# Kernel tuning notes

Measured on AMD Instinct MI355X. Metric: run time of the kernel, lower is better.

The kernel has to match this reference:

```python
import jax, jax.numpy as jnp
import numpy as np

D_MODEL = 512
N_HEADS = 8
DH = D_MODEL // N_HEADS            # 64
Q_PROJ = D_MODEL // 2              # 256
KV_PROJ = (2 * D_MODEL) // 3       # 341
ROPE_DIM = D_MODEL // 8            # 64 total rope dims
R = ROPE_DIM // N_HEADS            # 8 rope dims per head
THETA = 10000.0
EPS = 1e-5
B, S = 2, 2048


def layernorm(x, g, b):
    m = jnp.mean(x, axis=-1, keepdims=True)
    v = jnp.var(x, axis=-1, keepdims=True)
    return (x - m) * jax.lax.rsqrt(v + EPS) * g + b


def rope_cos_sin(seq_len, dtype):
    inv_freq = THETA ** (-jnp.arange(0, R, 2, dtype=jnp.float32) / R)   # (R/2,)
    ang = jnp.arange(seq_len, dtype=jnp.float32)[:, None] * inv_freq   # (S, R/2)
    cos = jnp.concatenate([jnp.cos(ang), jnp.cos(ang)], axis=-1)        # (S, R)
    sin = jnp.concatenate([jnp.sin(ang), jnp.sin(ang)], axis=-1)
    return cos.astype(dtype), sin.astype(dtype)


def apply_rope(x, cos, sin):
    # x: (B, H, S, R); neox-style half rotation
    x1, x2 = jnp.split(x, 2, axis=-1)
    rot = jnp.concatenate([-x2, x1], axis=-1)
    return x * cos + rot * sin


def setup_inputs() -> dict:
    key = jax.random.key(0)
    ks = jax.random.split(key, 9)
    p = lambda k, shape: 0.01 * jax.random.normal(k, shape, jnp.float32)
    return {
        "x": jax.random.normal(ks[0], (B, S, D_MODEL), jnp.float32),
        "W_dq": p(ks[1], (D_MODEL, Q_PROJ)),
        "W_uq": p(ks[2], (Q_PROJ, D_MODEL)),
        "W_qr": p(ks[3], (Q_PROJ, ROPE_DIM)),
        "W_dkv": p(ks[4], (D_MODEL, KV_PROJ)),
        "W_ukv": p(ks[5], (KV_PROJ, 2 * D_MODEL)),
        "W_kr": p(ks[6], (D_MODEL, ROPE_DIM)),
        "W_o": p(ks[7], (D_MODEL, D_MODEL)),
        "q_ln_g": jnp.ones((Q_PROJ,), jnp.float32),
        "q_ln_b": jnp.zeros((Q_PROJ,), jnp.float32),
        "kv_ln_g": jnp.ones((KV_PROJ,), jnp.float32),
        "kv_ln_b": jnp.zeros((KV_PROJ,), jnp.float32),
    }


def reference(x, W_dq, W_uq, W_qr, W_dkv, W_ukv, W_kr, W_o,
              q_ln_g, q_ln_b, kv_ln_g, kv_ln_b):
    b, s, d = x.shape
    # --- low-rank Q path ---
    cq = layernorm(x @ W_dq, q_ln_g, q_ln_b)                      # (B,S,Q_PROJ)
    Q = (cq @ W_uq).reshape(b, s, N_HEADS, DH).transpose(0, 2, 1, 3)
    Qr = (cq @ W_qr).reshape(b, s, N_HEADS, R).transpose(0, 2, 1, 3)
    cos, sin = rope_cos_sin(s, x.dtype)
    Qr = apply_rope(Qr, cos, sin)
    q = jnp.concatenate([Q, Qr], axis=-1)                          # (B,H,S,DH+R)
    # --- low-rank KV path ---
    ckv = layernorm(x @ W_dkv, kv_ln_g, kv_ln_b)                  # (B,S,KV_PROJ)
    KV = ckv @ W_ukv                                              # (B,S,2*D)
    K, V = KV[..., :D_MODEL], KV[..., D_MODEL:]
    K = K.reshape(b, s, N_HEADS, DH).transpose(0, 2, 1, 3)
    Kr = (x @ W_kr).reshape(b, s, N_HEADS, R).transpose(0, 2, 1, 3)
    Kr = apply_rope(Kr, cos, sin)
    k = jnp.concatenate([K, Kr], axis=-1)                          # (B,H,S,DH+R)
    v = V.reshape(b, s, N_HEADS, DH).transpose(0, 2, 1, 3)         # (B,H,S,DH)
    # --- causal SDPA ---
    scale = 1.0 / jnp.sqrt(jnp.asarray(DH + R, x.dtype))
    scores = jnp.einsum('bhqd,bhkd->bhqk', q, k) * scale           # (B,H,S,S)
    mask = jnp.tril(jnp.ones((s, s), dtype=bool))
    scores = jnp.where(mask, scores, jnp.finfo(scores.dtype).min)
    attn = jax.nn.softmax(scores, axis=-1)
    out = jnp.einsum('bhqk,bhkd->bhqd', attn, v)
    out = out.transpose(0, 2, 1, 3).reshape(b, s, d)
    return out @ W_o.T, ckv
```

## Files before the change

kernel.cpp:

```cpp
#include <hip/hip_runtime.h>
#include <hip/hip_bf16.h>

#define BATCH 2
#define SEQ 2048
#define DM 512
#define NH 8
#define DHD 64
#define QP 256
#define KVP 341
#define DQKPAD 96
#define MROWS 4096

#define OFF_X     0
#define OFF_WO    2932224
#define OFF_QG    3194368
#define OFF_QB    3194624
#define OFF_KG    3194880
#define OFF_KB    3195221

#define T_DQ   0
#define T_DKV  131072
#define T_KR   327680
#define T_UQ   360448
#define T_QR   491520
#define T_UKV  507904
#define T_TOT  901120

#define NW_X   2097152
#define NW_WO  262144
#define NW_PAR 1194

#define G_X   262144
#define G_WO  32768
#define G_PAR 150
#define G_WT  112640
#define G_TOT (G_X + G_WO + G_PAR + G_WT)

#define NSPLIT 8

typedef __bf16 bf16x8 __attribute__((ext_vector_type(8)));
typedef float f32x4 __attribute__((ext_vector_type(4)));
typedef __hip_bfloat16 bf16;
typedef unsigned short u16;

static __device__ __forceinline__ bf16x8 ld_bf8(const bf16* p) {
    return __builtin_bit_cast(bf16x8, *(const uint4*)p);
}

#define GL16(gp, lp) __builtin_amdgcn_global_load_lds( \
    (const __attribute__((address_space(1))) void*)(gp), \
    (__attribute__((address_space(3))) void*)(lp), 16, 0, 0)

__global__ __launch_bounds__(256) void prep(
    const void* px, const void* pwdq, const void* pwuq, const void* pwqr,
    const void* pwdkv, const void* pwukv, const void* pwkr, const void* pwo,
    const void* pqg, const void* pqb, const void* pkg, const void* pkb,
    u16* __restrict__ arena, u16* __restrict__ WT, int* __restrict__ flagp)
{
    __shared__ int cnt;
    if (threadIdx.x == 0) cnt = 0;
    __syncthreads();
    int bad = 0;
    const u16* xs = (const u16*)px;
    for (int i = threadIdx.x; i < 2048; i += 256) {
        u16 u = xs[i];
        int e = (u >> 7) & 0xFF;
        if (u != 0 && (e < 90 || e > 164)) bad++;
    }
    #pragma unroll
    for (int m2 = 1; m2 < 64; m2 <<= 1) bad += __shfl_xor(bad, m2);
    if ((threadIdx.x & 63) == 0) atomicAdd(&cnt, bad);
    __syncthreads();
    const int f = (cnt > 256) ? 1 : 0;
    if (blockIdx.x == 0 && threadIdx.x == 0) *flagp = f;

    int gid = blockIdx.x * 256 + threadIdx.x;
    if (gid >= G_TOT) return;

    auto rdu = [&](const void* s, int i) -> u16 {
        if (f) return __builtin_bit_cast(u16, __float2bfloat16(((const float*)s)[i]));
        return ((const u16*)s)[i];
    };

    if (gid < G_X + G_WO) {
        const void* src = (gid < G_X) ? px : pwo;
        int base = (gid < G_X) ? OFF_X : OFF_WO;
        int i = (gid < G_X) ? gid : gid - G_X;
        u16 out[8];
        if (f) {
            const float* s = (const float*)src + i * 8;
            #pragma unroll
            for (int j = 0; j < 8; ++j) out[j] = __builtin_bit_cast(u16, __float2bfloat16(s[j]));
        } else {
            *(uint4*)out = ((const uint4*)src)[i];
        }
        *(uint4*)&arena[base + i * 8] = *(uint4*)out;
    } else if (gid < G_X + G_WO + G_PAR) {
        int i0 = (gid - G_X - G_WO) * 8;
        for (int j = 0; j < 8; ++j) {
            int i = i0 + j;
            if (i >= NW_PAR) break;
            if (i < 256)      arena[OFF_QG + i]         = rdu(pqg, i);
            else if (i < 512) arena[OFF_QB + (i - 256)] = rdu(pqb, i - 256);
            else if (i < 853) arena[OFF_KG + (i - 512)] = rdu(pkg, i - 512);
            else              arena[OFF_KB + (i - 853)] = rdu(pkb, i - 853);
        }
    } else {
        int loc = (gid - (G_X + G_WO + G_PAR)) * 8;
        const void* src; int n, k0, sN, klim, nok;
        if (loc < T_DKV)      { int l = loc;          n = l >> 9; k0 = l & 511; src = pwdq;  sN = 256;  klim = 512; nok = 1; }
        else if (loc < T_KR)  { int l = loc - T_DKV;  n = l >> 9; k0 = l & 511; src = pwdkv; sN = 341;  klim = 512; nok = (n < 341); }
        else if (loc < T_UQ)  { int l = loc - T_KR;   n = l >> 9; k0 = l & 511; src = pwkr;  sN = 64;   klim = 512; nok = 1; }
        else if (loc < T_QR)  { int l = loc - T_UQ;   n = l >> 8; k0 = l & 255; src = pwuq;  sN = 512;  klim = 256; nok = 1; }
        else if (loc < T_UKV) { int l = loc - T_QR;   n = l >> 8; k0 = l & 255; src = pwqr;  sN = 64;   klim = 256; nok = 1; }
        else                  { int l = loc - T_UKV;  n = l / 384; k0 = l % 384; src = pwukv; sN = 1024; klim = 341; nok = 1; }
        u16 out[8];
        #pragma unroll
        for (int j = 0; j < 8; ++j) {
            int k = k0 + j;
            out[j] = (nok && k < klim) ? rdu(src, k * sN + n) : (u16)0;
        }
        *(uint4*)&WT[loc] = *(uint4*)out;
    }
}

static __device__ __forceinline__ void rope_epi(
    f32x4 (&acc)[2][4], bf16* __restrict__ dst, int m0, int w, int g, int lr, int tid, bool scaleq)
{
    const float SCv = 0.11785113019775793f;
    #pragma unroll
    for (int mt = 0; mt < 2; ++mt)
    #pragma unroll
    for (int r = 0; r < 4; ++r) {
        int gm = m0 + w * 32 + mt * 16 + g * 4 + r;
        int s = gm & 2047, b = gm >> 11;
        float ang = (float)s * exp2f(-(float)(lr & 3) * 3.3219280948873623f);
        float sn, cs;
        sincosf(ang, &sn, &cs);
        #pragma unroll
        for (int nt = 0; nt < 4; ++nt) {
            float v = acc[mt][nt][r];
            float pt = __shfl_xor(v, 4);
            float o = (lr & 4) ? fmaf(pt, sn, v * cs) : fmaf(-pt, sn, v * cs);
            if (scaleq) o *= SCv;
            int h = (nt * 16 + lr) >> 3, j = lr & 7;
            dst[((size_t)(b * NH + h) * SEQ + s) * DQKPAD + 64 + j] = __float2bfloat16(o);
        }
    }
    for (int u = tid; u < 128 * 96; u += 256) {
        int rw = u / 96, rem = u - rw * 96;
        int h = rem / 12, c = rem - h * 12;
        int row = m0 + rw, b2 = row >> 11, s2 = row & 2047;
        *(unsigned int*)&dst[((size_t)(b2 * NH + h) * SEQ + s2) * DQKPAD + 72 + c * 2] = 0u;
    }
}

__global__ __launch_bounds__(256) void gemm128(
    const bf16* __restrict__ A, int lda,
    const bf16* __restrict__ BT, int ldb,
    int N, int Kpad, int mode,
    void* __restrict__ C0, int ldc,
    bf16* __restrict__ kv_k, bf16* __restrict__ kv_v,
    const int* __restrict__ flagp, float* __restrict__ C0f)
{
    __shared__ __align__(16) bf16 LB[128 * 64 + 64 * 64];
    bf16* Al = LB;
    bf16* Bl = LB + 128 * 64;
    const int tid = threadIdx.x;
    const int m0 = blockIdx.y * 128, n0 = blockIdx.x * 64;
    const int lane = tid & 63, w = tid >> 6;
    const int g = lane >> 4, lr = lane & 15;
    f32x4 acc[2][4] = {};
    const int r8 = lane >> 3;
    const int xr8 = ((lane & 7) ^ r8) * 8;
    const int swx = (lr & 7) << 4;

    for (int k0 = 0; k0 < Kpad; k0 += 64) {
        #pragma unroll
        for (int i = 0; i < 4; ++i)
            GL16(&A[(size_t)(m0 + w * 32 + i * 8 + r8) * lda + k0 + xr8],
                 (char*)Al + w * 4096 + i * 1024);
        #pragma unroll
        for (int i = 0; i < 2; ++i)
            GL16(&BT[(size_t)(n0 + w * 16 + i * 8 + r8) * ldb + k0 + xr8],
                 (char*)Bl + w * 2048 + i * 1024);
        __syncthreads();
        #pragma unroll
        for (int ks = 0; ks < 2; ++ks) {
            const int cs = (ks * 64 + g * 16) ^ swx;
            bf16x8 a0 = ld_bf8((const bf16*)((const char*)Al + (w * 32 + lr) * 128 + cs));
            bf16x8 a1 = ld_bf8((const bf16*)((const char*)Al + (w * 32 + 16 + lr) * 128 + cs));
            #pragma unroll
            for (int nt = 0; nt < 4; ++nt) {
                bf16x8 b = ld_bf8((const bf16*)((const char*)Bl + (nt * 16 + lr) * 128 + cs));
                acc[0][nt] = __builtin_amdgcn_mfma_f32_16x16x32_bf16(a0, b, acc[0][nt], 0, 0, 0);
                acc[1][nt] = __builtin_amdgcn_mfma_f32_16x16x32_bf16(a1, b, acc[1][nt], 0, 0, 0);
            }
        }
        __syncthreads();
    }

    if (mode == 0 && n0 == 640) {
        rope_epi(acc, kv_k, m0, w, g, lr, tid, false);
        return;
    }
    if (mode == 4 && n0 == DM) {
        rope_epi(acc, (bf16*)C0, m0, w, g, lr, tid, true);
        return;
    }
    if (mode == 3 && n0 >= DM) {
        const int h = (n0 - DM) >> 6;
        const int b = m0 >> 11, s0 = m0 & 2047;
        bf16* T = LB;
        #pragma unroll
        for (int mt = 0; mt < 2; ++mt)
        #pragma unroll
        for (int nt = 0; nt < 4; ++nt)
        #pragma unroll
        for (int r = 0; r < 4; ++r) {
            int dv = nt * 16 + lr;
            int sl = w * 32 + mt * 16 + g * 4 + r;
            T[dv * 136 + sl] = __float2bfloat16(acc[mt][nt][r]);
        }
        __syncthreads();
        const int row = tid >> 2, coff = (tid & 3) * 32;
        bf16* dst = &kv_v[((size_t)(b * NH + h) * DHD + row) * SEQ + s0 + coff];
        const bf16* srcp = &T[row * 136 + coff];
        #pragma unroll
        for (int q2 = 0; q2 < 4; ++q2)
            *(uint4*)(dst + q2 * 8) = *(const uint4*)(srcp + q2 * 8);
        return;
    }

    const float SCv = 0.11785113019775793f;
    const int f32o = (mode == 1 && flagp) ? *flagp : 0;
    #pragma unroll
    for (int mt = 0; mt < 2; ++mt)
    #pragma unroll
    for (int nt = 0; nt < 4; ++nt)
    #pragma unroll
    for (int r = 0; r < 4; ++r) {
        int gm = m0 + w * 32 + mt * 16 + g * 4 + r;
        int gn = n0 + nt * 16 + lr;
        float v = acc[mt][nt][r];
        if (mode == 0) {
            ((float*)C0)[(size_t)gm * ldc + gn] = v;
        } else if (mode == 1) {
            if (f32o) C0f[(size_t)gm * ldc + gn] = v;
            else ((bf16*)C0)[(size_t)gm * ldc + gn] = __float2bfloat16(v);
        } else if (mode == 4) {
            int b = gm >> 11, s = gm & 2047;
            int h = gn >> 6, dh = gn & 63;
            ((bf16*)C0)[((size_t)(b * NH + h) * SEQ + s) * DQKPAD + dh] = __float2bfloat16(v * SCv);
        } else {
            int b = gm >> 11, s = gm & 2047;
            int h = gn >> 6, dh = gn & 63;
            kv_k[((size_t)(b * NH + h) * SEQ + s) * DQKPAD + dh] = __float2bfloat16(v);
        }
    }
}

__global__ __launch_bounds__(256) void ln_both(
    const float* __restrict__ y,
    const bf16* __restrict__ qg, const bf16* __restrict__ qb,
    const bf16* __restrict__ kg, const bf16* __restrict__ kb,
    bf16* __restrict__ cq, bf16* __restrict__ ckv_b, float* __restrict__ ckv_f,
    bf16* __restrict__ ckvp, const int* __restrict__ flagp)
{
    const int w = threadIdx.x >> 6, lane = threadIdx.x & 63;
    const int blk = blockIdx.x;
    if (blk < 1024) {
        const int row = blk * 4 + w;
        const float* yr = y + (size_t)row * 704;
        float s = 0.f, ss = 0.f;
        for (int i = lane; i < 256; i += 64) { float v = yr[i]; s += v; ss += v * v; }
        #pragma unroll
        for (int m = 1; m < 64; m <<= 1) { s += __shfl_xor(s, m); ss += __shfl_xor(ss, m); }
        float mean = s * (1.f / 256.f);
        float var = ss * (1.f / 256.f) - mean * mean;
        float rstd = rsqrtf(var + 1e-5f);
        for (int i = lane; i < 256; i += 64) {
            float v = (yr[i] - mean) * rstd * __bfloat162float(qg[i]) + __bfloat162float(qb[i]);
            cq[(size_t)row * 256 + i] = __float2bfloat16(v);
        }
    } else {
        const int row = (blk - 1024) * 4 + w;
        const float* yr = y + (size_t)row * 704 + 256;
        const int f32o = *flagp;
        float s = 0.f, ss = 0.f;
        for (int i = lane; i < KVP; i += 64) { float v = yr[i]; s += v; ss += v * v; }
        #pragma unroll
        for (int m = 1; m < 64; m <<= 1) { s += __shfl_xor(s, m); ss += __shfl_xor(ss, m); }
        float mean = s * (1.f / 341.f);
        float var = ss * (1.f / 341.f) - mean * mean;
        float rstd = rsqrtf(var + 1e-5f);
        for (int i = lane; i < KVP; i += 64) {
            float v = (yr[i] - mean) * rstd * __bfloat162float(kg[i]) + __bfloat162float(kb[i]);
            if (f32o) ckv_f[(size_t)row * KVP + i] = v;
            else ckv_b[(size_t)row * KVP + i] = __float2bfloat16(v);
            ckvp[(size_t)row * 384 + i] = __float2bfloat16(v);
        }
        for (int i = KVP + lane; i < 384; i += 64) ckvp[(size_t)row * 384 + i] = __float2bfloat16(0.f);
    }
}

__global__ __launch_bounds__(256) void attn_split3(
    const bf16* __restrict__ qa, const bf16* __restrict__ ka, const bf16* __restrict__ vat,
    bf16* __restrict__ po, float* __restrict__ mlm, float* __restrict__ mll)
{
    __shared__ __align__(16) bf16 Kl[64][104];
    __shared__ __align__(16) bf16 Vt[64][72];
    __shared__ __align__(16) bf16 Pl[4][16][72];
    const int sp = blockIdx.x, pr = blockIdx.y, bh = blockIdx.z;
    const int tid = threadIdx.x, w = tid >> 6, lane = tid & 63;
    const int g = lane >> 4, lr = lane & 15;
    const size_t base = (size_t)bh * SEQ;
    const float L2E = 1.4426950408889634f;
    const bf16* vb = vat + (size_t)bh * DHD * SEQ;

    for (int half = 0; half < 2; ++half) {
        const int qb = half ? (31 - pr) : pr;
        const int qrow0 = qb * 64 + w * 16;
        const int myq = qrow0 + lr;

        bf16x8 qf[3];
        #pragma unroll
        for (int kc = 0; kc < 3; ++kc)
            qf[kc] = ld_bf8(&qa[(base + myq) * DQKPAD + kc * 32 + g * 8]);

        float m_p = -1e30f, l_p = 0.f;
        f32x4 acc_o[4] = {};
        const int ng = qb + 1;
        const int bs = (ng * sp) >> 3, be = (ng * (sp + 1)) >> 3;

        for (int gi = bs; gi < be; ++gi) {
            const int j0 = gi * 64;
            __syncthreads();
            for (int u = tid; u < 768; u += 256) {
                int row = u / 12, cc = (u % 12) * 8;
                *(uint4*)&Kl[row][cc] = *(const uint4*)&ka[(base + j0 + row) * DQKPAD + cc];
            }
            {
                int d = tid >> 2, ko = (tid & 3) * 16;
                const bf16* vsrc = &vb[(size_t)d * SEQ + j0 + ko];
                *(uint4*)&Vt[d][ko]     = *(const uint4*)vsrc;
                *(uint4*)&Vt[d][ko + 8] = *(const uint4*)(vsrc + 8);
            }
            __syncthreads();

            f32x4 accs[4] = {};
            #pragma unroll
            for (int kc = 0; kc < 3; ++kc) {
                #pragma unroll
                for (int nt = 0; nt < 4; ++nt) {
                    bf16x8 kf = ld_bf8(&Kl[nt * 16 + lr][kc * 32 + g * 8]);
                    accs[nt] = __builtin_amdgcn_mfma_f32_16x16x32_bf16(kf, qf[kc], accs[nt], 0, 0, 0);
                }
            }
            float s_[4][4];
            float mloc = -1e30f;
            if (j0 + 63 > qrow0) {
                #pragma unroll
                for (int nt = 0; nt < 4; ++nt)
                #pragma unroll
                for (int r = 0; r < 4; ++r) {
                    int key = j0 + nt * 16 + g * 4 + r;
                    float sv = accs[nt][r];
                    sv = (key <= myq) ? sv : -1e30f;
                    s_[nt][r] = sv;
                    mloc = fmaxf(mloc, sv);
                }
            } else {
                #pragma unroll
                for (int nt = 0; nt < 4; ++nt)
                #pragma unroll
                for (int r = 0; r < 4; ++r) {
                    float sv = accs[nt][r];
                    s_[nt][r] = sv;
                    mloc = fmaxf(mloc, sv);
                }
            }
            mloc = fmaxf(mloc, __shfl_xor(mloc, 16));
            mloc = fmaxf(mloc, __shfl_xor(mloc, 32));

            if (__all(mloc <= m_p + 8.f)) {
                float rs = 0.f;
                #pragma unroll
                for (int nt = 0; nt < 4; ++nt)
                #pragma unroll
                for (int r = 0; r < 4; ++r) {
                    float p = exp2f((s_[nt][r] - m_p) * L2E);
                    s_[nt][r] = p; rs += p;
                }
                rs += __shfl_xor(rs, 16);
                rs += __shfl_xor(rs, 32);
                l_p += rs;
            } else {
                float mn = fmaxf(m_p, mloc);
                float alpha = exp2f((m_p - mn) * L2E);
                m_p = mn;
                float rs = 0.f;
                #pragma unroll
                for (int nt = 0; nt < 4; ++nt)
                #pragma unroll
                for (int r = 0; r < 4; ++r) {
                    float p = exp2f((s_[nt][r] - mn) * L2E);
                    s_[nt][r] = p; rs += p;
                }
                rs += __shfl_xor(rs, 16);
                rs += __shfl_xor(rs, 32);
                l_p = l_p * alpha + rs;
                float ar[4];
                #pragma unroll
                for (int r = 0; r < 4; ++r) ar[r] = __shfl(alpha, g * 4 + r);
                #pragma unroll
                for (int nv = 0; nv < 4; ++nv)
                #pragma unroll
                for (int r = 0; r < 4; ++r) acc_o[nv][r] *= ar[r];
            }
            #pragma unroll
            for (int nt = 0; nt < 4; ++nt) {
                ushort4 pk;
                pk.x = __builtin_bit_cast(u16, __float2bfloat16(s_[nt][0]));
                pk.y = __builtin_bit_cast(u16, __float2bfloat16(s_[nt][1]));
                pk.z = __builtin_bit_cast(u16, __float2bfloat16(s_[nt][2]));
                pk.w = __builtin_bit_cast(u16, __float2bfloat16(s_[nt][3]));
                *(ushort4*)&Pl[w][lr][nt * 16 + g * 4] = pk;
            }
            bf16x8 pf0 = ld_bf8(&Pl[w][lr][g * 8]);
            bf16x8 pf1 = ld_bf8(&Pl[w][lr][32 + g * 8]);
            #pragma unroll
            for (int nv = 0; nv < 4; ++nv) {
                bf16x8 vf0 = ld_bf8(&Vt[nv * 16 + lr][g * 8]);
                acc_o[nv] = __builtin_amdgcn_mfma_f32_16x16x32_bf16(pf0, vf0, acc_o[nv], 0, 0, 0);
                bf16x8 vf1 = ld_bf8(&Vt[nv * 16 + lr][32 + g * 8]);
                acc_o[nv] = __builtin_amdgcn_mfma_f32_16x16x32_bf16(pf1, vf1, acc_o[nv], 0, 0, 0);
            }
        }

        const size_t pb = (size_t)(bh * NSPLIT + sp) * SEQ;
        #pragma unroll
        for (int r = 0; r < 4; ++r) {
            int qrow = qrow0 + g * 4 + r;
            #pragma unroll
            for (int nv = 0; nv < 4; ++nv)
                po[(pb + qrow) * DHD + nv * 16 + lr] = __float2bfloat16(acc_o[nv][r]);
        }
        if (lane < 16) {
            mlm[pb + qrow0 + lane] = m_p;
            mll[pb + qrow0 + lane] = l_p;
        }
    }
}

__global__ __launch_bounds__(256) void attn_combine(
    const bf16* __restrict__ po, const float* __restrict__ mlm, const float* __restrict__ mll,
    bf16* __restrict__ ao)
{
    int id = blockIdx.x * 256 + threadIdx.x;
    int bh = id >> 14;
    int rem = id & 16383;
    int q = rem >> 3, dc = (rem & 7) * 8;
    const float L2E = 1.4426950408889634f;
    size_t mlb = (size_t)bh * NSPLIT * SEQ + q;
    float ms[NSPLIT], ls[NSPLIT];
    #pragma unroll
    for (int s = 0; s < NSPLIT; ++s) { ms[s] = mlm[mlb + (size_t)s * SEQ]; ls[s] = mll[mlb + (size_t)s * SEQ]; }
    float M = -1e30f;
    #pragma unroll
    for (int s = 0; s < NSPLIT; ++s) M = fmaxf(M, ms[s]);
    float wsc[NSPLIT]; float L = 0.f;
    #pragma unroll
    for (int s = 0; s < NSPLIT; ++s) { wsc[s] = exp2f((ms[s] - M) * L2E); L += wsc[s] * ls[s]; }
    float o[8] = {};
    #pragma unroll
    for (int s = 0; s < NSPLIT; ++s) {
        if (ls[s] <= 0.f) continue;
        bf16x8 pv = ld_bf8(&po[((size_t)(bh * NSPLIT + s) * SEQ + q) * DHD + dc]);
        #pragma unroll
        for (int j = 0; j < 8; ++j) o[j] += wsc[s] * (float)pv[j];
    }
    float invL = 1.f / L;
    int b = bh >> 3, h = bh & 7;
    __bf16 tmp[8];
    #pragma unroll
    for (int j = 0; j < 8; ++j) tmp[j] = (__bf16)(o[j] * invL);
    *(uint4*)&ao[((size_t)(b * SEQ) + q) * DM + h * DHD + dc] = *(uint4*)tmp;
}

extern "C" void kernel_launch(void* const* d_in, const int* in_sizes, int n_in,
                              void* d_out, int out_size, void* d_ws, size_t ws_size,
                              hipStream_t stream) {
    char* ws = (char*)d_ws;
    bf16* AR      = (bf16*)(ws + 0);
    float* ml_m   = (float*)(ws + 0);
    float* ml_l   = (float*)(ws + 1048576);
    bf16* WT      = (bf16*)(ws + 6391296);
    int*  flagp   = (int*)(ws + 8193536);
    float* y      = (float*)(ws + 8194048);
    bf16* cq      = (bf16*)(ws + 19728384);
    bf16* ckvp    = (bf16*)(ws + 21825536);
    bf16* q_attn  = (bf16*)(ws + 26019840);
    bf16* k_attn  = (bf16*)(ws + 32311296);
    bf16* v_attnT = (bf16*)(ws + 38602752);
    bf16* attn_o  = (bf16*)(ws + 42797056);
    bf16* po      = (bf16*)(ws + 50331648);

    const bf16* xb  = AR + OFF_X;
    const bf16* W_o = AR + OFF_WO;
    const bf16* qg  = AR + OFF_QG;
    const bf16* qb_ = AR + OFF_QB;
    const bf16* kg  = AR + OFF_KG;
    const bf16* kb  = AR + OFF_KB;

    bf16*  out_b = (bf16*)d_out;
    float* out_f = (float*)d_out;
    bf16*  ckv_b = out_b + (size_t)MROWS * DM;
    float* ckv_f = out_f + (size_t)MROWS * DM;

    dim3 blk(256);
    prep<<<dim3((G_TOT + 255) / 256), blk, 0, stream>>>(
        d_in[0], d_in[1], d_in[2], d_in[3], d_in[4], d_in[5],
        d_in[6], d_in[7], d_in[8], d_in[9], d_in[10], d_in[11],
        (u16*)AR, (u16*)WT, flagp);
    gemm128<<<dim3(11, 32), blk, 0, stream>>>(xb, DM, WT + T_DQ, DM, 704, DM, 0, y, 704, k_attn, nullptr, nullptr, nullptr);
    ln_both<<<dim3(2048), blk, 0, stream>>>(y, qg, qb_, kg, kb, cq, ckv_b, ckv_f, ckvp, flagp);
    gemm128<<<dim3(9, 32), blk, 0, stream>>>(cq, QP, WT + T_UQ, QP, 576, QP, 4, q_attn, 0, nullptr, nullptr, nullptr, nullptr);
    gemm128<<<dim3(16, 32), blk, 0, stream>>>(ckvp, 384, WT + T_UKV, 384, 1024, 384, 3, nullptr, 0, k_attn, v_attnT, nullptr, nullptr);
    attn_split3<<<dim3(NSPLIT, 16, 16), blk, 0, stream>>>(q_attn, k_attn, v_attnT, po, ml_m, ml_l);
    attn_combine<<<dim3(1024), blk, 0, stream>>>(po, ml_m, ml_l, attn_o);
    gemm128<<<dim3(8, 32), blk, 0, stream>>>(attn_o, DM, W_o, DM, DM, DM, 1, out_b, DM, nullptr, nullptr, flagp, out_f);
}
```

Before: 126.3 us.

## Rewrite attention with 32x32 MFMA, register-resident P, swizzled LDS, 128-row tiles

The attention kernel moves from 16x16x32 MFMA on 64-query tiles to 32x32x16 MFMA on 128-query tiles with 32 queries per wave. P is kept in registers via packed bf16 conversion and permlane32 swaps instead of a round trip through LDS. K and V tiles use an XOR swizzle in place of padding to avoid bank conflicts. The KV split count drops from 8 to 4 and fully masked tiles are skipped per wave. This cuts LDS traffic and instruction count, at the cost of fewer blocks, which lowers parallelism and changes load balance.

```diff
diff --git a/kernel.cpp b/kernel.cpp
--- a/kernel.cpp
+++ b/kernel.cpp
@@ -36,15 +36,22 @@
 #define G_WT  112640
 #define G_TOT (G_X + G_WO + G_PAR + G_WT)
 
-#define NSPLIT 8
+#define NSPLIT 4
 
 typedef __bf16 bf16x8 __attribute__((ext_vector_type(8)));
 typedef float f32x4 __attribute__((ext_vector_type(4)));
+typedef float f32x16 __attribute__((ext_vector_type(16)));
 typedef __hip_bfloat16 bf16;
 typedef unsigned short u16;
+typedef unsigned int u32;
 
 static __device__ __forceinline__ bf16x8 ld_bf8(const bf16* p) {
     return __builtin_bit_cast(bf16x8, *(const uint4*)p);
+}
+static __device__ __forceinline__ u32 cvtpk(float lo, float hi) {
+    u32 r;
+    asm("v_cvt_pk_bf16_f32 %0, %1, %2" : "=v"(r) : "v"(lo), "v"(hi));
+    return r;
 }
 
 #define GL16(gp, lp) __builtin_amdgcn_global_load_lds( \
@@ -304,95 +311,80 @@
     }
 }
 
-__global__ __launch_bounds__(256) void attn_split3(
+__global__ __launch_bounds__(256) void attn_v4(
     const bf16* __restrict__ qa, const bf16* __restrict__ ka, const bf16* __restrict__ vat,
     bf16* __restrict__ po, float* __restrict__ mlm, float* __restrict__ mll)
 {
-    __shared__ __align__(16) bf16 Kl[64][104];
-    __shared__ __align__(16) bf16 Vt[64][72];
-    __shared__ __align__(16) bf16 Pl[4][16][72];
+    __shared__ __align__(16) bf16 Kl[64][128];
+    __shared__ __align__(16) bf16 Vt[64][128];
     const int sp = blockIdx.x, pr = blockIdx.y, bh = blockIdx.z;
     const int tid = threadIdx.x, w = tid >> 6, lane = tid & 63;
-    const int g = lane >> 4, lr = lane & 15;
+    const int q31 = lane & 31, h = lane >> 5, q15 = lane & 15;
     const size_t base = (size_t)bh * SEQ;
     const float L2E = 1.4426950408889634f;
     const bf16* vb = vat + (size_t)bh * DHD * SEQ;
 
     for (int half = 0; half < 2; ++half) {
-        const int qb = half ? (31 - pr) : pr;
-        const int qrow0 = qb * 64 + w * 16;
-        const int myq = qrow0 + lr;
-
-        bf16x8 qf[3];
-        #pragma unroll
-        for (int kc = 0; kc < 3; ++kc)
-            qf[kc] = ld_bf8(&qa[(base + myq) * DQKPAD + kc * 32 + g * 8]);
+        const int t = half ? (15 - pr) : pr;
+        const int tb = t * 128;
+        const int qrow0w = tb + w * 32;
+        const int myq = qrow0w + q31;
+
+        bf16x8 qf[6];
+        #pragma unroll
+        for (int ks = 0; ks < 6; ++ks)
+            qf[ks] = ld_bf8(&qa[(base + myq) * DQKPAD + ks * 16 + h * 8]);
 
         float m_p = -1e30f, l_p = 0.f;
-        f32x4 acc_o[4] = {};
-        const int ng = qb + 1;
-        const int bs = (ng * sp) >> 3, be = (ng * (sp + 1)) >> 3;
+        f32x16 acc_o0 = {}, acc_o1 = {};
+        const int G = 2 * (t + 1);
+        const int bs = (G * sp) >> 2, be = (G * (sp + 1)) >> 2;
 
         for (int gi = bs; gi < be; ++gi) {
             const int j0 = gi * 64;
             __syncthreads();
             for (int u = tid; u < 768; u += 256) {
-                int row = u / 12, cc = (u % 12) * 8;
-                *(uint4*)&Kl[row][cc] = *(const uint4*)&ka[(base + j0 + row) * DQKPAD + cc];
-            }
-            {
-                int d = tid >> 2, ko = (tid & 3) * 16;
-                const bf16* vsrc = &vb[(size_t)d * SEQ + j0 + ko];
-                *(uint4*)&Vt[d][ko]     = *(const uint4*)vsrc;
-                *(uint4*)&Vt[d][ko + 8] = *(const uint4*)(vsrc + 8);
+                int row = u / 12, sl = u % 12;
+                *(uint4*)&Kl[row][(sl ^ (row & 15)) * 8] =
+                    *(const uint4*)&ka[(base + j0 + row) * DQKPAD + sl * 8];
+            }
+            for (int u = tid; u < 512; u += 256) {
+                int d = u >> 3, sl = u & 7;
+                *(uint4*)&Vt[d][(sl ^ (d & 15)) * 8] =
+                    *(const uint4*)&vb[(size_t)d * SEQ + j0 + sl * 8];
             }
             __syncthreads();
-
-            f32x4 accs[4] = {};
+            if (j0 > qrow0w + 31) continue;
+
+            f32x16 accs0 = {}, accs1 = {};
             #pragma unroll
-            for (int kc = 0; kc < 3; ++kc) {
-                #pragma unroll
-                for (int nt = 0; nt < 4; ++nt) {
-                    bf16x8 kf = ld_bf8(&Kl[nt * 16 + lr][kc * 32 + g * 8]);
-                    accs[nt] = __builtin_amdgcn_mfma_f32_16x16x32_bf16(kf, qf[kc], accs[nt], 0, 0, 0);
+            for (int ks = 0; ks < 6; ++ks) {
+                bf16x8 kf0 = ld_bf8(&Kl[q31][(((ks * 2 + h) ^ q15) * 8)]);
+                bf16x8 kf1 = ld_bf8(&Kl[32 + q31][(((ks * 2 + h) ^ q15) * 8)]);
+                accs0 = __builtin_amdgcn_mfma_f32_32x32x16_bf16(kf0, qf[ks], accs0, 0, 0, 0);
+                accs1 = __builtin_amdgcn_mfma_f32_32x32x16_bf16(kf1, qf[ks], accs1, 0, 0, 0);
+            }
+            float mloc = -1e30f;
+            const bool diag = (j0 + 63 > qrow0w);
+            #pragma unroll
+            for (int r = 0; r < 16; ++r) {
+                int rowk = (r & 3) + 8 * (r >> 2) + 4 * h;
+                if (diag) {
+                    if (j0 + rowk > myq) accs0[r] = -1e30f;
+                    if (j0 + 32 + rowk > myq) accs1[r] = -1e30f;
                 }
-            }
-            float s_[4][4];
-            float mloc = -1e30f;
-            if (j0 + 63 > qrow0) {
-                #pragma unroll
-                for (int nt = 0; nt < 4; ++nt)
-                #pragma unroll
-                for (int r = 0; r < 4; ++r) {
-                    int key = j0 + nt * 16 + g * 4 + r;
-                    float sv = accs[nt][r];
-                    sv = (key <= myq) ? sv : -1e30f;
-                    s_[nt][r] = sv;
-                    mloc = fmaxf(mloc, sv);
-                }
-            } else {
-                #pragma unroll
-                for (int nt = 0; nt < 4; ++nt)
-                #pragma unroll
-                for (int r = 0; r < 4; ++r) {
-                    float sv = accs[nt][r];
-                    s_[nt][r] = sv;
-                    mloc = fmaxf(mloc, sv);
-                }
-            }
-            mloc = fmaxf(mloc, __shfl_xor(mloc, 16));
+                mloc = fmaxf(mloc, fmaxf(accs0[r], accs1[r]));
+            }
             mloc = fmaxf(mloc, __shfl_xor(mloc, 32));
 
             if (__all(mloc <= m_p + 8.f)) {
                 float rs = 0.f;
                 #pragma unroll
-                for (int nt = 0; nt < 4; ++nt)
-                #pragma unroll
-                for (int r = 0; r < 4; ++r) {
-                    float p = exp2f((s_[nt][r] - m_p) * L2E);
-                    s_[nt][r] = p; rs += p;
+                for (int r = 0; r < 16; ++r) {
+                    float p0 = exp2f((accs0[r] - m_p) * L2E);
+                    float p1 = exp2f((accs1[r] - m_p) * L2E);
+                    accs0[r] = p0; accs1[r] = p1; rs += p0 + p1;
                 }
-                rs += __shfl_xor(rs, 16);
                 rs += __shfl_xor(rs, 32);
                 l_p += rs;
             } else {
@@ -401,54 +393,56 @@
                 m_p = mn;
                 float rs = 0.f;
                 #pragma unroll
-                for (int nt = 0; nt < 4; ++nt)
-                #pragma unroll
-                for (int r = 0; r < 4; ++r) {
-                    float p = exp2f((s_[nt][r] - mn) * L2E);
-                    s_[nt][r] = p; rs += p;
+                for (int r = 0; r < 16; ++r) {
+                    float p0 = exp2f((accs0[r] - mn) * L2E);
+                    float p1 = exp2f((accs1[r] - mn) * L2E);
+                    accs0[r] = p0; accs1[r] = p1; rs += p0 + p1;
                 }
-                rs += __shfl_xor(rs, 16);
                 rs += __shfl_xor(rs, 32);
                 l_p = l_p * alpha + rs;
-                float ar[4];
                 #pragma unroll
-                for (int r = 0; r < 4; ++r) ar[r] = __shfl(alpha, g * 4 + r);
+                for (int r = 0; r < 16; ++r) {
+                    float ar = __shfl(alpha, (r & 3) + 8 * (r >> 2) + 4 * h);
+                    acc_o0[r] *= ar; acc_o1[r] *= ar;
+                }
+            }
+
+            bf16x8 pa[4];
+            #pragma unroll
+            for (int kt = 0; kt < 2; ++kt) {
+                u32 U[8];
                 #pragma unroll
-                for (int nv = 0; nv < 4; ++nv)
-                #pragma unroll
-                for (int r = 0; r < 4; ++r) acc_o[nv][r] *= ar[r];
+                for (int u = 0; u < 8; ++u)
+                    U[u] = kt == 0 ? cvtpk(accs0[2 * u], accs0[2 * u + 1])
+                                   : cvtpk(accs1[2 * u], accs1[2 * u + 1]);
+                asm volatile("v_permlane32_swap_b32 %0, %1" : "+v"(U[0]), "+v"(U[2]));
+                asm volatile("v_permlane32_swap_b32 %0, %1" : "+v"(U[1]), "+v"(U[3]));
+                asm volatile("v_permlane32_swap_b32 %0, %1" : "+v"(U[4]), "+v"(U[6]));
+                asm volatile("v_permlane32_swap_b32 %0, %1" : "+v"(U[5]), "+v"(U[7]));
+                u32 w0[4] = {U[0], U[1], U[2], U[3]};
+                u32 w1[4] = {U[4], U[5], U[6], U[7]};
+                pa[kt * 2]     = __builtin_bit_cast(bf16x8, *(uint4*)w0);
+                pa[kt * 2 + 1] = __builtin_bit_cast(bf16x8, *(uint4*)w1);
             }
             #pragma unroll
-            for (int nt = 0; nt < 4; ++nt) {
-                ushort4 pk;
-                pk.x = __builtin_bit_cast(u16, __float2bfloat16(s_[nt][0]));
-                pk.y = __builtin_bit_cast(u16, __float2bfloat16(s_[nt][1]));
-                pk.z = __builtin_bit_cast(u16, __float2bfloat16(s_[nt][2]));
-                pk.w = __builtin_bit_cast(u16, __float2bfloat16(s_[nt][3]));
-                *(ushort4*)&Pl[w][lr][nt * 16 + g * 4] = pk;
-            }
-            bf16x8 pf0 = ld_bf8(&Pl[w][lr][g * 8]);
-            bf16x8 pf1 = ld_bf8(&Pl[w][lr][32 + g * 8]);
-            #pragma unroll
-            for (int nv = 0; nv < 4; ++nv) {
-                bf16x8 vf0 = ld_bf8(&Vt[nv * 16 + lr][g * 8]);
-                acc_o[nv] = __builtin_amdgcn_mfma_f32_16x16x32_bf16(pf0, vf0, acc_o[nv], 0, 0, 0);
-                bf16x8 vf1 = ld_bf8(&Vt[nv * 16 + lr][32 + g * 8]);
-                acc_o[nv] = __builtin_amdgcn_mfma_f32_16x16x32_bf16(pf1, vf1, acc_o[nv], 0, 0, 0);
+            for (int ksv = 0; ksv < 4; ++ksv) {
+                bf16x8 vf0 = ld_bf8(&Vt[q31][(((ksv * 2 + h) ^ q15) * 8)]);
+                bf16x8 vf1 = ld_bf8(&Vt[32 + q31][(((ksv * 2 + h) ^ q15) * 8)]);
+                acc_o0 = __builtin_amdgcn_mfma_f32_32x32x16_bf16(pa[ksv], vf0, acc_o0, 0, 0, 0);
+                acc_o1 = __builtin_amdgcn_mfma_f32_32x32x16_bf16(pa[ksv], vf1, acc_o1, 0, 0, 0);
             }
         }
 
         const size_t pb = (size_t)(bh * NSPLIT + sp) * SEQ;
         #pragma unroll
-        for (int r = 0; r < 4; ++r) {
-            int qrow = qrow0 + g * 4 + r;
-            #pragma unroll
-            for (int nv = 0; nv < 4; ++nv)
-                po[(pb + qrow) * DHD + nv * 16 + lr] = __float2bfloat16(acc_o[nv][r]);
-        }
-        if (lane < 16) {
-            mlm[pb + qrow0 + lane] = m_p;
-            mll[pb + qrow0 + lane] = l_p;
+        for (int r = 0; r < 16; ++r) {
+            int q = qrow0w + (r & 3) + 8 * (r >> 2) + 4 * h;
+            po[(pb + q) * DHD + q31] = __float2bfloat16(acc_o0[r]);
+            po[(pb + q) * DHD + 32 + q31] = __float2bfloat16(acc_o1[r]);
+        }
+        if (lane < 32) {
+            mlm[pb + qrow0w + lane] = m_p;
+            mll[pb + qrow0w + lane] = l_p;
         }
     }
 }
@@ -527,7 +521,7 @@
     ln_both<<<dim3(2048), blk, 0, stream>>>(y, qg, qb_, kg, kb, cq, ckv_b, ckv_f, ckvp, flagp);
     gemm128<<<dim3(9, 32), blk, 0, stream>>>(cq, QP, WT + T_UQ, QP, 576, QP, 4, q_attn, 0, nullptr, nullptr, nullptr, nullptr);
     gemm128<<<dim3(16, 32), blk, 0, stream>>>(ckvp, 384, WT + T_UKV, 384, 1024, 384, 3, nullptr, 0, k_attn, v_attnT, nullptr, nullptr);
-    attn_split3<<<dim3(NSPLIT, 16, 16), blk, 0, stream>>>(q_attn, k_attn, v_attnT, po, ml_m, ml_l);
+    attn_v4<<<dim3(NSPLIT, 8, 16), blk, 0, stream>>>(q_attn, k_attn, v_attnT, po, ml_m, ml_l);
     attn_combine<<<dim3(1024), blk, 0, stream>>>(po, ml_m, ml_l, attn_o);
     gemm128<<<dim3(8, 32), blk, 0, stream>>>(attn_o, DM, W_o, DM, DM, DM, 1, out_b, DM, nullptr, nullptr, flagp, out_f);
 }
```

New measurement: 177.6 us. +40.6%, slower.
